# Performance work log

Hardware: AMD Instinct MI355X
Metric: run time of the kernel (lower is better)

The kernel has to match this reference:

```python
import jax, jax.numpy as jnp
import numpy as np
from jax import lax

B = 32      # point clouds per batch
P = 1024    # points per cloud (equal-sized, contiguous in batch vector)
K = 20      # kNN neighbors (includes self, as in PyG knn)
N = B * P


def _w(key, fan_in, fan_out):
    return jax.random.normal(key, (fan_in, fan_out), dtype=jnp.float32) / np.sqrt(fan_in)


def setup_inputs() -> dict:
    key = jax.random.key(0)
    ks = jax.random.split(key, 12)
    return {
        "pos": jax.random.normal(ks[0], (N, 3), dtype=jnp.float32),
        "batch": jnp.repeat(jnp.arange(B, dtype=jnp.int32), P),
        # conv1 MLP([6,64,64]): Linear(6,64)+BN+ReLU, Linear(64,64) plain
        "conv1_W1": _w(ks[1], 6, 64),
        "conv1_b1": jnp.zeros((64,), jnp.float32),
        "conv1_bn_scale": jnp.ones((64,), jnp.float32),   # BN eval folded affine
        "conv1_bn_bias": jnp.zeros((64,), jnp.float32),
        "conv1_W2": _w(ks[2], 64, 64),
        "conv1_b2": jnp.zeros((64,), jnp.float32),
        # conv2 MLP([128,128]): single plain Linear(128,128)
        "conv2_W": _w(ks[3], 128, 128),
        "conv2_b": jnp.zeros((128,), jnp.float32),
        # lin: Linear(64+128, 128)
        "lin_W": _w(ks[4], 192, 128),
        "lin_b": jnp.zeros((128,), jnp.float32),
    }


def _edge_conv(x, mlp_fn):
    # x: [B, P, d]. Dynamic kNN in feature space per cloud, edge MLP, max-aggregate.
    sq = jnp.sum(x * x, axis=-1)                                  # [B,P]
    dist = sq[:, :, None] - 2.0 * jnp.einsum('bpd,bqd->bpq', x, x) + sq[:, None, :]
    _, idx = lax.top_k(-dist, K)                                  # [B,P,K] nearest (incl. self)
    x_j = jax.vmap(lambda xb, ib: xb[ib])(x, idx)                 # [B,P,K,d] gather neighbors
    x_i = jnp.broadcast_to(x[:, :, None, :], x_j.shape)
    e = jnp.concatenate([x_i, x_j - x_i], axis=-1)                # [B,P,K,2d]
    return jnp.max(mlp_fn(e), axis=2)                             # max aggregation -> [B,P,out]


def reference(pos, batch, conv1_W1, conv1_b1, conv1_bn_scale, conv1_bn_bias,
              conv1_W2, conv1_b2, conv2_W, conv2_b, lin_W, lin_b):
    x = pos.reshape(B, P, 3)

    def mlp1(e):
        h = e @ conv1_W1 + conv1_b1
        h = jax.nn.relu(h * conv1_bn_scale + conv1_bn_bias)       # BN(eval) + ReLU
        return h @ conv1_W2 + conv1_b2                            # plain last layer

    def mlp2(e):
        return e @ conv2_W + conv2_b                              # plain single layer

    x1 = _edge_conv(x, mlp1)                                      # [B,P,64]
    x2 = _edge_conv(x1, mlp2)                                     # [B,P,128]
    h = jnp.concatenate([x1, x2], axis=-1) @ lin_W + lin_b        # [B,P,128]
    # global_max_pool over each cloud via batch ids
    out = jax.ops.segment_max(h.reshape(N, 128), batch, num_segments=B)
    return out                                                    # [B,128]
```

## Files before the change

kernel.cpp:

```cpp
#include <hip/hip_runtime.h>
#include <math.h>

#define NPTS 32768
#define NB 32
#define PP 1024
#define KK 20

using bf16x8 = __attribute__((ext_vector_type(8))) short;
using f32x4 = __attribute__((ext_vector_type(4))) float;

constexpr size_t OFF_X1 = 0;
constexpr size_t OFF_IDX = OFF_X1 + (size_t)NPTS * 64 * 4;
constexpr size_t OFF_U = OFF_IDX + (size_t)NPTS * KK * 4;
constexpr size_t OFF_V = OFF_U + (size_t)NPTS * 128 * 4;
constexpr size_t OFF_X2 = OFF_V + (size_t)NPTS * 128 * 4;
constexpr size_t OFF_H = OFF_X2 + (size_t)NPTS * 128 * 4;
constexpr size_t OFF_PART = OFF_H + (size_t)NPTS * 128 * 4;
constexpr size_t OFF_SQN = OFF_PART + (size_t)32 * 8 * 128 * 4;

__device__ __forceinline__ void topk_insert(unsigned (&l)[KK], unsigned key) {
#pragma unroll
  for (int j = KK - 1; j >= 1; --j) {
    unsigned r;
    asm("v_med3_u32 %0, %1, %2, %3" : "=v"(r) : "v"(key), "v"(l[j - 1]), "v"(l[j]));
    l[j] = r;
  }
  l[0] = key < l[0] ? key : l[0];
}

__device__ __forceinline__ unsigned pack_key(float dist, int q) {
  return (__float_as_uint(dist) & 0xFFFFFC00u) | (unsigned)q;
}

__device__ __forceinline__ void split_bf16(float x, short& hi, short& lo) {
  unsigned u = __float_as_uint(x);
  hi = (short)(u >> 16);
  float fh = __uint_as_float(u & 0xFFFF0000u);
  float r = x - fh;
  lo = (short)(__float_as_uint(r) >> 16);
}

template <int S>
__global__ __launch_bounds__(256, 4) void knn_topk3(const float* __restrict__ x,
                                                    unsigned* __restrict__ pk) {
  constexpr int CH = PP / S;
  __shared__ __align__(16) float xs[1024];
  __shared__ __align__(16) float ys[1024];
  __shared__ __align__(16) float zs[1024];
  int bx = blockIdx.x;
  int s = bx % S;
  int tile = (bx / S) % (PP / 256);
  int b = bx / (S * (PP / 256));
  int tid = threadIdx.x;
  const float* xb = x + (size_t)b * PP * 3;

  for (int t = tid; t < 768; t += 256) {
    float4 v = ((const float4*)xb)[t];
    int e = 4 * t;
    float vals[4] = {v.x, v.y, v.z, v.w};
#pragma unroll
    for (int j = 0; j < 4; ++j) {
      int p = (e + j) / 3, d = (e + j) % 3;
      if (d == 0) xs[p] = vals[j];
      else if (d == 1) ys[p] = vals[j];
      else zs[p] = vals[j];
    }
  }
  __syncthreads();

  int i = tile * 256 + tid;
  float xi0 = xs[i], xi1 = ys[i], xi2 = zs[i];

  unsigned l[KK];
#pragma unroll
  for (int j = 0; j < KK; ++j) l[j] = 0xFFFFFFFFu;

  int q0 = s * CH;
  float4 qx = *(const float4*)&xs[q0];
  float4 qy = *(const float4*)&ys[q0];
  float4 qz = *(const float4*)&zs[q0];
  for (int c = 0; c < CH; c += 4) {
    int qm = (q0 + c + 4) & 1023;
    float4 nqx = *(const float4*)&xs[qm];
    float4 nqy = *(const float4*)&ys[qm];
    float4 nqz = *(const float4*)&zs[qm];
    float cx[4] = {qx.x, qx.y, qx.z, qx.w};
    float cy[4] = {qy.x, qy.y, qy.z, qy.w};
    float cz[4] = {qz.x, qz.y, qz.z, qz.w};
#pragma unroll
    for (int j = 0; j < 4; ++j) {
      float d0 = xi0 - cx[j], d1 = xi1 - cy[j], d2 = xi2 - cz[j];
      float dist = fmaf(d0, d0, fmaf(d1, d1, d2 * d2));
      topk_insert(l, pack_key(dist, q0 + c + j));
    }
    qx = nqx; qy = nqy; qz = nqz;
  }
  size_t base = ((size_t)b * PP + i) * S + s;
#pragma unroll
  for (int j = 0; j < KK; ++j) pk[base * KK + j] = l[j];
}

template <int S>
__global__ __launch_bounds__(256) void knn_merge(const unsigned* __restrict__ pk,
                                                 int* __restrict__ idx_out) {
  int p = blockIdx.x * 256 + threadIdx.x;
  const unsigned* g = pk + (size_t)p * S * KK;
  unsigned l[KK];
#pragma unroll
  for (int j = 0; j < KK; ++j) l[j] = g[j];
  for (int s = 1; s < S; ++s) {
    const unsigned* gs = g + s * KK;
#pragma unroll
    for (int j = 0; j < KK; ++j) topk_insert(l, gs[j]);
  }
#pragma unroll
  for (int j = 0; j < KK; ++j) idx_out[(size_t)p * KK + j] = (int)(l[j] & 1023u);
}

__global__ __launch_bounds__(256) void precompute1(const float* __restrict__ pos,
                                                   const float* __restrict__ W1,
                                                   const float* __restrict__ b1,
                                                   float* __restrict__ u1,
                                                   float* __restrict__ v1) {
  int gid = blockIdx.x * 256 + threadIdx.x;
  int i = gid >> 6, c = gid & 63;
  float p0 = pos[(size_t)i * 3 + 0], p1 = pos[(size_t)i * 3 + 1], p2 = pos[(size_t)i * 3 + 2];
  float a0 = W1[0 * 64 + c], a1 = W1[1 * 64 + c], a2 = W1[2 * 64 + c];
  float g0 = W1[3 * 64 + c], g1 = W1[4 * 64 + c], g2 = W1[5 * 64 + c];
  float v = fmaf(p0, g0, fmaf(p1, g1, p2 * g2));
  float u = b1[c];
  u = fmaf(p0, a0 - g0, u);
  u = fmaf(p1, a1 - g1, u);
  u = fmaf(p2, a2 - g2, u);
  u1[gid] = u;
  v1[gid] = v;
}

__global__ __launch_bounds__(256) void edge_conv1_mfma(
    const float* __restrict__ u1, const float* __restrict__ v1,
    const int* __restrict__ idx, const float* __restrict__ W2,
    const float* __restrict__ scale, const float* __restrict__ bias,
    const float* __restrict__ b2,
    short* __restrict__ x1hl, float* __restrict__ sqn) {
  __shared__ float Cs[160 * 68];
  __shared__ int jt[160];
  __shared__ float xs[512];
  int tid = threadIdx.x;
  int p0 = blockIdx.x * 8;
  int b = p0 >> 10;
  if (tid < 160) {
    int e = tid;
    int i = p0 + e / 20;
    jt[e] = (b << 10) + idx[(size_t)i * KK + e % 20];
  }
  int w = tid >> 6, l = tid & 63, quad = l >> 4, lm = l & 15;
  int kq = quad * 8;
  float4 s00 = *(const float4*)(scale + kq);
  float4 s01 = *(const float4*)(scale + kq + 4);
  float4 s10 = *(const float4*)(scale + 32 + kq);
  float4 s11 = *(const float4*)(scale + 32 + kq + 4);
  float4 c00 = *(const float4*)(bias + kq);
  float4 c01 = *(const float4*)(bias + kq + 4);
  float4 c10 = *(const float4*)(bias + 32 + kq);
  float4 c11 = *(const float4*)(bias + 32 + kq + 4);
  bf16x8 Bh[4][2], Bl[4][2];
#pragma unroll
  for (int nt = 0; nt < 4; ++nt) {
#pragma unroll
    for (int ks = 0; ks < 2; ++ks) {
#pragma unroll
      for (int jj = 0; jj < 8; ++jj) {
        float wv = W2[(size_t)(ks * 32 + kq + jj) * 64 + nt * 16 + lm];
        short hi, lo;
        split_bf16(wv, hi, lo);
        Bh[nt][ks][jj] = hi;
        Bl[nt][ks][jj] = lo;
      }
    }
  }
  __syncthreads();

  for (int s = w; s < 10; s += 4) {
    f32x4 acc[4];
#pragma unroll
    for (int nt = 0; nt < 4; ++nt) acc[nt] = (f32x4){0.f, 0.f, 0.f, 0.f};
    int e = s * 16 + lm;
    int p = e / 20;
    int jrow = jt[e];
    const float* urow = u1 + (size_t)(p0 + p) * 64;
    const float* vrow = v1 + (size_t)jrow * 64;
#pragma unroll
    for (int ks = 0; ks < 2; ++ks) {
      int koff = ks * 32 + kq;
      float4 va = *(const float4*)(vrow + koff);
      float4 vb = *(const float4*)(vrow + koff + 4);
      float4 ua = *(const float4*)(urow + koff);
      float4 ub = *(const float4*)(urow + koff + 4);
      float4 sA = ks ? s10 : s00, sB = ks ? s11 : s01;
      float4 cA = ks ? c10 : c00, cB = ks ? c11 : c01;
      float hv[8];
      hv[0] = fmaxf(fmaf(ua.x + va.x, sA.x, cA.x), 0.f);
      hv[1] = fmaxf(fmaf(ua.y + va.y, sA.y, cA.y), 0.f);
      hv[2] = fmaxf(fmaf(ua.z + va.z, sA.z, cA.z), 0.f);
      hv[3] = fmaxf(fmaf(ua.w + va.w, sA.w, cA.w), 0.f);
      hv[4] = fmaxf(fmaf(ub.x + vb.x, sB.x, cB.x), 0.f);
      hv[5] = fmaxf(fmaf(ub.y + vb.y, sB.y, cB.y), 0.f);
      hv[6] = fmaxf(fmaf(ub.z + vb.z, sB.z, cB.z), 0.f);
      hv[7] = fmaxf(fmaf(ub.w + vb.w, sB.w, cB.w), 0.f);
      bf16x8 Ah, Al;
#pragma unroll
      for (int jj = 0; jj < 8; ++jj) {
        short hi, lo;
        split_bf16(hv[jj], hi, lo);
        Ah[jj] = hi;
        Al[jj] = lo;
      }
#pragma unroll
      for (int nt = 0; nt < 4; ++nt) {
        acc[nt] = __builtin_amdgcn_mfma_f32_16x16x32_bf16(Ah, Bh[nt][ks], acc[nt], 0, 0, 0);
        acc[nt] = __builtin_amdgcn_mfma_f32_16x16x32_bf16(Al, Bh[nt][ks], acc[nt], 0, 0, 0);
        acc[nt] = __builtin_amdgcn_mfma_f32_16x16x32_bf16(Ah, Bl[nt][ks], acc[nt], 0, 0, 0);
      }
    }
#pragma unroll
    for (int nt = 0; nt < 4; ++nt) {
#pragma unroll
      for (int r = 0; r < 4; ++r) {
        Cs[(size_t)(s * 16 + quad * 4 + r) * 68 + nt * 16 + lm] = acc[nt][r];
      }
    }
  }
  __syncthreads();
  for (int o = tid; o < 512; o += 256) {
    int p = o >> 6, c = o & 63;
    float m = -__builtin_inff();
    for (int k = 0; k < KK; ++k) m = fmaxf(m, Cs[(size_t)(p * 20 + k) * 68 + c]);
    m += b2[c];
    size_t gi = (size_t)(p0 + p) * 128 + c;
    short hi, lo;
    split_bf16(m, hi, lo);
    x1hl[gi] = hi;
    x1hl[gi + 64] = lo;
    xs[o] = m;
  }
  __syncthreads();
  if (tid < 8) {
    float ss = 0.f;
    for (int c = 0; c < 64; ++c) {
      float v = xs[tid * 64 + c];
      ss = fmaf(v, v, ss);
    }
    sqn[p0 + tid] = ss;
  }
}

__global__ __launch_bounds__(256, 4) void knn2_mfma(const short* __restrict__ x1hl,
                                                    const float* __restrict__ sqn,
                                                    unsigned* __restrict__ pk) {
  __shared__ float sqs[1024];
  int bx = blockIdx.x;
  int s = bx & 1;
  int pb = bx >> 1;
  int p0 = pb * 64;
  int b = p0 >> 10;
  int tid = threadIdx.x;
  for (int t = tid; t < 1024; t += 256) sqs[t] = sqn[(size_t)b * PP + t];
  int w = tid >> 6, l = tid & 63, quad = l >> 4, lm = l & 15;
  size_t gi = (size_t)p0 + w * 16 + lm;
  const short* brow = x1hl + gi * 128 + quad * 8;
  bf16x8 Bh0 = *(const bf16x8*)(brow);
  bf16x8 Bl0 = *(const bf16x8*)(brow + 64);
  bf16x8 Bh1 = *(const bf16x8*)(brow + 32);
  bf16x8 Bl1 = *(const bf16x8*)(brow + 96);
  float sqi = sqn[gi];
  __syncthreads();
  unsigned list[KK];
#pragma unroll
  for (int j = 0; j < KK; ++j) list[j] = 0xFFFFFFFFu;

  const size_t cbase = (size_t)b * PP;
  int m0 = s * 512;
  const short* arow = x1hl + (cbase + m0 + lm) * 128 + quad * 8;
  bf16x8 Ah0 = *(const bf16x8*)(arow);
  bf16x8 Al0 = *(const bf16x8*)(arow + 64);
  bf16x8 Ah1 = *(const bf16x8*)(arow + 32);
  bf16x8 Al1 = *(const bf16x8*)(arow + 96);
  float sq0 = sqs[m0 + quad * 4 + 0];
  float sq1 = sqs[m0 + quad * 4 + 1];
  float sq2 = sqs[m0 + quad * 4 + 2];
  float sq3 = sqs[m0 + quad * 4 + 3];

  for (int it = 0; it < 32; ++it) {
    int m0n = (m0 + 16) & 1023;
    const short* arn = x1hl + (cbase + m0n + lm) * 128 + quad * 8;
    bf16x8 nAh0 = *(const bf16x8*)(arn);
    bf16x8 nAl0 = *(const bf16x8*)(arn + 64);
    bf16x8 nAh1 = *(const bf16x8*)(arn + 32);
    bf16x8 nAl1 = *(const bf16x8*)(arn + 96);
    float nsq0 = sqs[m0n + quad * 4 + 0];
    float nsq1 = sqs[m0n + quad * 4 + 1];
    float nsq2 = sqs[m0n + quad * 4 + 2];
    float nsq3 = sqs[m0n + quad * 4 + 3];

    f32x4 acc = (f32x4){0.f, 0.f, 0.f, 0.f};
    acc = __builtin_amdgcn_mfma_f32_16x16x32_bf16(Ah0, Bh0, acc, 0, 0, 0);
    acc = __builtin_amdgcn_mfma_f32_16x16x32_bf16(Al0, Bh0, acc, 0, 0, 0);
    acc = __builtin_amdgcn_mfma_f32_16x16x32_bf16(Ah0, Bl0, acc, 0, 0, 0);
    acc = __builtin_amdgcn_mfma_f32_16x16x32_bf16(Ah1, Bh1, acc, 0, 0, 0);
    acc = __builtin_amdgcn_mfma_f32_16x16x32_bf16(Al1, Bh1, acc, 0, 0, 0);
    acc = __builtin_amdgcn_mfma_f32_16x16x32_bf16(Ah1, Bl1, acc, 0, 0, 0);

    int qb = m0 + quad * 4;
    float d0 = fmaxf(0.f, fmaf(-2.f, acc[0], sqi + sq0));
    topk_insert(list, pack_key(d0, qb + 0));
    float d1 = fmaxf(0.f, fmaf(-2.f, acc[1], sqi + sq1));
    topk_insert(list, pack_key(d1, qb + 1));
    float d2 = fmaxf(0.f, fmaf(-2.f, acc[2], sqi + sq2));
    topk_insert(list, pack_key(d2, qb + 2));
    float d3 = fmaxf(0.f, fmaf(-2.f, acc[3], sqi + sq3));
    topk_insert(list, pack_key(d3, qb + 3));

    Ah0 = nAh0; Al0 = nAl0; Ah1 = nAh1; Al1 = nAl1;
    sq0 = nsq0; sq1 = nsq1; sq2 = nsq2; sq3 = nsq3;
    m0 += 16;
  }
  unsigned sub = s * 4 + quad;
  unsigned* dst = pk + ((size_t)gi * 8 + sub) * KK;
#pragma unroll
  for (int j = 0; j < KK; ++j) dst[j] = list[j];
}

__global__ __launch_bounds__(256) void pre2_mfma(const short* __restrict__ x1hl,
                                                 const float* __restrict__ cW,
                                                 const float* __restrict__ cb,
                                                 float* __restrict__ u2,
                                                 float* __restrict__ v2) {
  constexpr int BS = 72;
  __shared__ short Bh[128 * BS];
  __shared__ short Bl[128 * BS];
  int tid = threadIdx.x;
  int nh = blockIdx.x & 1;
  int p0 = (blockIdx.x >> 1) * 64;
  for (int t = tid; t < 64 * 128; t += 256) {
    int k = t >> 7, n = t & 127;
    float wb_ = cW[(size_t)(64 + k) * 128 + n];
    float wv = nh ? wb_ : (cW[(size_t)k * 128 + n] - wb_);
    short hi, lo;
    split_bf16(wv, hi, lo);
    Bh[n * BS + k] = hi;
    Bl[n * BS + k] = lo;
  }
  __syncthreads();
  int w = tid >> 6, l = tid & 63, quad = l >> 4, lm = l & 15;
  int row = p0 + w * 16 + lm;
  f32x4 acc[8];
#pragma unroll
  for (int nt = 0; nt < 8; ++nt) acc[nt] = (f32x4){0.f, 0.f, 0.f, 0.f};
#pragma unroll
  for (int ks = 0; ks < 2; ++ks) {
    int kb = ks * 32 + quad * 8;
    bf16x8 Ah = *(const bf16x8*)(x1hl + (size_t)row * 128 + kb);
    bf16x8 Al = *(const bf16x8*)(x1hl + (size_t)row * 128 + 64 + kb);
#pragma unroll
    for (int nt = 0; nt < 8; ++nt) {
      bf16x8 Wh = *(const bf16x8*)(Bh + (nt * 16 + lm) * BS + kb);
      bf16x8 Wl = *(const bf16x8*)(Bl + (nt * 16 + lm) * BS + kb);
      acc[nt] = __builtin_amdgcn_mfma_f32_16x16x32_bf16(Ah, Wh, acc[nt], 0, 0, 0);
      acc[nt] = __builtin_amdgcn_mfma_f32_16x16x32_bf16(Al, Wh, acc[nt], 0, 0, 0);
      acc[nt] = __builtin_amdgcn_mfma_f32_16x16x32_bf16(Ah, Wl, acc[nt], 0, 0, 0);
    }
  }
  float* out = nh ? v2 : u2;
  int prow = p0 + w * 16 + quad * 4;
#pragma unroll
  for (int nt = 0; nt < 8; ++nt) {
    int col = nt * 16 + lm;
    float bias = nh ? 0.f : cb[col];
#pragma unroll
    for (int r = 0; r < 4; ++r)
      out[(size_t)(prow + r) * 128 + col] = acc[nt][r] + bias;
  }
}

__global__ __launch_bounds__(256) void gathermax2(const float* __restrict__ u2,
                                                  const float* __restrict__ v2,
                                                  const int* __restrict__ idx,
                                                  short* __restrict__ x2hl) {
  int gid = blockIdx.x * 256 + threadIdx.x;
  int i = gid >> 7, c = gid & 127;
  int b = i >> 10;
  const int* myidx = idx + (size_t)i * KK;
  float m = -__builtin_inff();
  for (int k = 0; k < KK; ++k) {
    int j = (b << 10) + myidx[k];
    m = fmaxf(m, v2[(size_t)j * 128 + c]);
  }
  float x = u2[gid] + m;
  short hi, lo;
  split_bf16(x, hi, lo);
  x2hl[(size_t)i * 256 + c] = hi;
  x2hl[(size_t)i * 256 + 128 + c] = lo;
}

__global__ __launch_bounds__(256) void lin_mfma(const short* __restrict__ x1hl,
                                                const short* __restrict__ x2hl,
                                                const float* __restrict__ LW,
                                                const float* __restrict__ lb,
                                                float* __restrict__ h) {
  constexpr int BS = 200;
  __shared__ short Bh[64 * BS];
  __shared__ short Bl[64 * BS];
  int tid = threadIdx.x;
  int nh = blockIdx.x & 1;
  int p0 = (blockIdx.x >> 1) * 64;
  for (int t = tid; t < 192 * 64; t += 256) {
    int k = t >> 6, n = t & 63;
    float wv = LW[(size_t)k * 128 + nh * 64 + n];
    short hi, lo;
    split_bf16(wv, hi, lo);
    Bh[n * BS + k] = hi;
    Bl[n * BS + k] = lo;
  }
  __syncthreads();
  int w = tid >> 6, l = tid & 63, quad = l >> 4, lm = l & 15;
  int row = p0 + w * 16 + lm;
  f32x4 acc[4];
#pragma unroll
  for (int nt = 0; nt < 4; ++nt) acc[nt] = (f32x4){0.f, 0.f, 0.f, 0.f};
#pragma unroll
  for (int ks = 0; ks < 6; ++ks) {
    int kb = ks * 32 + quad * 8;
    bf16x8 Ah, Al;
    if (ks < 2) {
      Ah = *(const bf16x8*)(x1hl + (size_t)row * 128 + kb);
      Al = *(const bf16x8*)(x1hl + (size_t)row * 128 + 64 + kb);
    } else {
      Ah = *(const bf16x8*)(x2hl + (size_t)row * 256 + (kb - 64));
      Al = *(const bf16x8*)(x2hl + (size_t)row * 256 + 128 + (kb - 64));
    }
#pragma unroll
    for (int nt = 0; nt < 4; ++nt) {
      bf16x8 Wh = *(const bf16x8*)(Bh + (nt * 16 + lm) * BS + kb);
      bf16x8 Wl = *(const bf16x8*)(Bl + (nt * 16 + lm) * BS + kb);
      acc[nt] = __builtin_amdgcn_mfma_f32_16x16x32_bf16(Ah, Wh, acc[nt], 0, 0, 0);
      acc[nt] = __builtin_amdgcn_mfma_f32_16x16x32_bf16(Al, Wh, acc[nt], 0, 0, 0);
      acc[nt] = __builtin_amdgcn_mfma_f32_16x16x32_bf16(Ah, Wl, acc[nt], 0, 0, 0);
    }
  }
  int prow = p0 + w * 16 + quad * 4;
#pragma unroll
  for (int nt = 0; nt < 4; ++nt) {
    int col = nh * 64 + nt * 16 + lm;
    float bias = lb[col];
#pragma unroll
    for (int r = 0; r < 4; ++r)
      h[(size_t)(prow + r) * 128 + col] = acc[nt][r] + bias;
  }
}

__global__ __launch_bounds__(128) void segmax_a(const float* __restrict__ h,
                                                float* __restrict__ part) {
  int b = blockIdx.x >> 3, chunk = blockIdx.x & 7;
  int c = threadIdx.x;
  float m = -__builtin_inff();
  for (int p = 0; p < 128; ++p) {
    size_t i = (size_t)b * PP + chunk * 128 + p;
    m = fmaxf(m, h[i * 128 + c]);
  }
  part[(size_t)blockIdx.x * 128 + c] = m;
}

__global__ __launch_bounds__(128) void segmax_b(const float* __restrict__ part,
                                                float* __restrict__ out) {
  int b = blockIdx.x;
  int c = threadIdx.x;
  float m = -__builtin_inff();
  for (int k = 0; k < 8; ++k) m = fmaxf(m, part[((size_t)b * 8 + k) * 128 + c]);
  out[(size_t)b * 128 + c] = m;
}

extern "C" void kernel_launch(void* const* d_in, const int* in_sizes, int n_in,
                              void* d_out, int out_size, void* d_ws, size_t ws_size,
                              hipStream_t stream) {
  const float* pos = (const float*)d_in[0];
  const float* W1 = (const float*)d_in[2];
  const float* b1 = (const float*)d_in[3];
  const float* bn_s = (const float*)d_in[4];
  const float* bn_b = (const float*)d_in[5];
  const float* W2 = (const float*)d_in[6];
  const float* b2 = (const float*)d_in[7];
  const float* cW = (const float*)d_in[8];
  const float* cb = (const float*)d_in[9];
  const float* LW = (const float*)d_in[10];
  const float* lb = (const float*)d_in[11];
  float* out = (float*)d_out;

  char* ws = (char*)d_ws;
  short* x1hl = (short*)(ws + OFF_X1);
  int* idx = (int*)(ws + OFF_IDX);
  float* u1 = (float*)(ws + OFF_U);
  float* v1 = (float*)(ws + OFF_V);
  float* u2 = (float*)(ws + OFF_U);
  float* v2 = (float*)(ws + OFF_V);
  short* x2hl = (short*)(ws + OFF_X2);
  float* hbuf = (float*)(ws + OFF_H);
  float* part = (float*)(ws + OFF_PART);
  float* sqn = (float*)(ws + OFF_SQN);
  unsigned* pk = (unsigned*)(ws + OFF_U);

  knn_topk3<8><<<NB * 4 * 8, 256, 0, stream>>>(pos, pk);
  knn_merge<8><<<NPTS / 256, 256, 0, stream>>>(pk, idx);
  precompute1<<<NPTS * 64 / 256, 256, 0, stream>>>(pos, W1, b1, u1, v1);
  edge_conv1_mfma<<<NPTS / 8, 256, 0, stream>>>(u1, v1, idx, W2, bn_s, bn_b, b2,
                                                x1hl, sqn);
  knn2_mfma<<<NPTS / 64 * 2, 256, 0, stream>>>(x1hl, sqn, pk);
  knn_merge<8><<<NPTS / 256, 256, 0, stream>>>(pk, idx);
  pre2_mfma<<<NPTS / 64 * 2, 256, 0, stream>>>(x1hl, cW, cb, u2, v2);
  gathermax2<<<NPTS * 128 / 256, 256, 0, stream>>>(u2, v2, idx, x2hl);
  lin_mfma<<<NPTS / 64 * 2, 256, 0, stream>>>(x1hl, x2hl, LW, lb, hbuf);
  segmax_a<<<NB * 8, 128, 0, stream>>>(hbuf, part);
  segmax_b<<<NB, 128, 0, stream>>>(part, out);
}
```

Measured before the change: 344.6 us.

## Split per-thread top-k into two independent lists and stage knn2 tiles in LDS

Both kNN kernels now keep two independent top-20 lists per thread, each fed alternate candidates. This breaks the serial med3 insertion dependency chain and gives the scheduler more instruction-level parallelism. knn2 stages 128-row bf16 hi/lo tiles of candidate features in shared memory instead of loading per-lane from global memory. The merge kernel now reduces 16 partial lists and exits early once a sorted partial list's next key cannot enter the current list. The costs are more registers, double the partial-list traffic and a longer merge.

```diff
diff --git a/kernel.cpp b/kernel.cpp
--- a/kernel.cpp
+++ b/kernel.cpp
@@ -71,9 +71,9 @@
   int i = tile * 256 + tid;
   float xi0 = xs[i], xi1 = ys[i], xi2 = zs[i];
 
-  unsigned l[KK];
-#pragma unroll
-  for (int j = 0; j < KK; ++j) l[j] = 0xFFFFFFFFu;
+  unsigned la[KK], lb[KK];
+#pragma unroll
+  for (int j = 0; j < KK; ++j) { la[j] = 0xFFFFFFFFu; lb[j] = 0xFFFFFFFFu; }
 
   int q0 = s * CH;
   float4 qx = *(const float4*)&xs[q0];
@@ -87,17 +87,29 @@
     float cx[4] = {qx.x, qx.y, qx.z, qx.w};
     float cy[4] = {qy.x, qy.y, qy.z, qy.w};
     float cz[4] = {qz.x, qz.y, qz.z, qz.w};
-#pragma unroll
-    for (int j = 0; j < 4; ++j) {
-      float d0 = xi0 - cx[j], d1 = xi1 - cy[j], d2 = xi2 - cz[j];
-      float dist = fmaf(d0, d0, fmaf(d1, d1, d2 * d2));
-      topk_insert(l, pack_key(dist, q0 + c + j));
+    {
+      float d0 = xi0 - cx[0], d1 = xi1 - cy[0], d2 = xi2 - cz[0];
+      topk_insert(la, pack_key(fmaf(d0, d0, fmaf(d1, d1, d2 * d2)), q0 + c + 0));
+    }
+    {
+      float d0 = xi0 - cx[2], d1 = xi1 - cy[2], d2 = xi2 - cz[2];
+      topk_insert(lb, pack_key(fmaf(d0, d0, fmaf(d1, d1, d2 * d2)), q0 + c + 2));
+    }
+    {
+      float d0 = xi0 - cx[1], d1 = xi1 - cy[1], d2 = xi2 - cz[1];
+      topk_insert(la, pack_key(fmaf(d0, d0, fmaf(d1, d1, d2 * d2)), q0 + c + 1));
+    }
+    {
+      float d0 = xi0 - cx[3], d1 = xi1 - cy[3], d2 = xi2 - cz[3];
+      topk_insert(lb, pack_key(fmaf(d0, d0, fmaf(d1, d1, d2 * d2)), q0 + c + 3));
     }
     qx = nqx; qy = nqy; qz = nqz;
   }
-  size_t base = ((size_t)b * PP + i) * S + s;
-#pragma unroll
-  for (int j = 0; j < KK; ++j) pk[base * KK + j] = l[j];
+  size_t base = ((size_t)b * PP + i) * (2 * S) + s * 2;
+#pragma unroll
+  for (int j = 0; j < KK; ++j) pk[base * KK + j] = la[j];
+#pragma unroll
+  for (int j = 0; j < KK; ++j) pk[(base + 1) * KK + j] = lb[j];
 }
 
 template <int S>
@@ -110,8 +122,11 @@
   for (int j = 0; j < KK; ++j) l[j] = g[j];
   for (int s = 1; s < S; ++s) {
     const unsigned* gs = g + s * KK;
-#pragma unroll
-    for (int j = 0; j < KK; ++j) topk_insert(l, gs[j]);
+    for (int j = 0; j < KK; ++j) {
+      unsigned key = gs[j];
+      if (key >= l[KK - 1]) break;
+      topk_insert(l, key);
+    }
   }
 #pragma unroll
   for (int j = 0; j < KK; ++j) idx_out[(size_t)p * KK + j] = (int)(l[j] & 1023u);
@@ -257,14 +272,17 @@
 __global__ __launch_bounds__(256, 4) void knn2_mfma(const short* __restrict__ x1hl,
                                                     const float* __restrict__ sqn,
                                                     unsigned* __restrict__ pk) {
-  __shared__ float sqs[1024];
+  constexpr int TS = 72;
+  __shared__ float sqs[512];
+  __shared__ __align__(16) short tileH[128 * TS];
+  __shared__ __align__(16) short tileL[128 * TS];
   int bx = blockIdx.x;
   int s = bx & 1;
   int pb = bx >> 1;
   int p0 = pb * 64;
   int b = p0 >> 10;
   int tid = threadIdx.x;
-  for (int t = tid; t < 1024; t += 256) sqs[t] = sqn[(size_t)b * PP + t];
+  for (int t = tid; t < 512; t += 256) sqs[t] = sqn[(size_t)b * PP + s * 512 + t];
   int w = tid >> 6, l = tid & 63, quad = l >> 4, lm = l & 15;
   size_t gi = (size_t)p0 + w * 16 + lm;
   const short* brow = x1hl + gi * 128 + quad * 8;
@@ -273,61 +291,61 @@
   bf16x8 Bh1 = *(const bf16x8*)(brow + 32);
   bf16x8 Bl1 = *(const bf16x8*)(brow + 96);
   float sqi = sqn[gi];
-  __syncthreads();
-  unsigned list[KK];
-#pragma unroll
-  for (int j = 0; j < KK; ++j) list[j] = 0xFFFFFFFFu;
-
-  const size_t cbase = (size_t)b * PP;
-  int m0 = s * 512;
-  const short* arow = x1hl + (cbase + m0 + lm) * 128 + quad * 8;
-  bf16x8 Ah0 = *(const bf16x8*)(arow);
-  bf16x8 Al0 = *(const bf16x8*)(arow + 64);
-  bf16x8 Ah1 = *(const bf16x8*)(arow + 32);
-  bf16x8 Al1 = *(const bf16x8*)(arow + 96);
-  float sq0 = sqs[m0 + quad * 4 + 0];
-  float sq1 = sqs[m0 + quad * 4 + 1];
-  float sq2 = sqs[m0 + quad * 4 + 2];
-  float sq3 = sqs[m0 + quad * 4 + 3];
-
-  for (int it = 0; it < 32; ++it) {
-    int m0n = (m0 + 16) & 1023;
-    const short* arn = x1hl + (cbase + m0n + lm) * 128 + quad * 8;
-    bf16x8 nAh0 = *(const bf16x8*)(arn);
-    bf16x8 nAl0 = *(const bf16x8*)(arn + 64);
-    bf16x8 nAh1 = *(const bf16x8*)(arn + 32);
-    bf16x8 nAl1 = *(const bf16x8*)(arn + 96);
-    float nsq0 = sqs[m0n + quad * 4 + 0];
-    float nsq1 = sqs[m0n + quad * 4 + 1];
-    float nsq2 = sqs[m0n + quad * 4 + 2];
-    float nsq3 = sqs[m0n + quad * 4 + 3];
-
-    f32x4 acc = (f32x4){0.f, 0.f, 0.f, 0.f};
-    acc = __builtin_amdgcn_mfma_f32_16x16x32_bf16(Ah0, Bh0, acc, 0, 0, 0);
-    acc = __builtin_amdgcn_mfma_f32_16x16x32_bf16(Al0, Bh0, acc, 0, 0, 0);
-    acc = __builtin_amdgcn_mfma_f32_16x16x32_bf16(Ah0, Bl0, acc, 0, 0, 0);
-    acc = __builtin_amdgcn_mfma_f32_16x16x32_bf16(Ah1, Bh1, acc, 0, 0, 0);
-    acc = __builtin_amdgcn_mfma_f32_16x16x32_bf16(Al1, Bh1, acc, 0, 0, 0);
-    acc = __builtin_amdgcn_mfma_f32_16x16x32_bf16(Ah1, Bl1, acc, 0, 0, 0);
-
-    int qb = m0 + quad * 4;
-    float d0 = fmaxf(0.f, fmaf(-2.f, acc[0], sqi + sq0));
-    topk_insert(list, pack_key(d0, qb + 0));
-    float d1 = fmaxf(0.f, fmaf(-2.f, acc[1], sqi + sq1));
-    topk_insert(list, pack_key(d1, qb + 1));
-    float d2 = fmaxf(0.f, fmaf(-2.f, acc[2], sqi + sq2));
-    topk_insert(list, pack_key(d2, qb + 2));
-    float d3 = fmaxf(0.f, fmaf(-2.f, acc[3], sqi + sq3));
-    topk_insert(list, pack_key(d3, qb + 3));
-
-    Ah0 = nAh0; Al0 = nAl0; Ah1 = nAh1; Al1 = nAl1;
-    sq0 = nsq0; sq1 = nsq1; sq2 = nsq2; sq3 = nsq3;
-    m0 += 16;
-  }
-  unsigned sub = s * 4 + quad;
-  unsigned* dst = pk + ((size_t)gi * 8 + sub) * KK;
-#pragma unroll
-  for (int j = 0; j < KK; ++j) dst[j] = list[j];
+
+  unsigned la[KK], lc[KK];
+#pragma unroll
+  for (int j = 0; j < KK; ++j) { la[j] = 0xFFFFFFFFu; lc[j] = 0xFFFFFFFFu; }
+
+  int rr = tid & 127, hh = tid >> 7;
+  short* dstT = (hh ? tileL : tileH) + rr * TS;
+  const size_t cbase = (size_t)b * PP + s * 512;
+  const short* srcbase = x1hl + (cbase + rr) * 128 + hh * 64;
+
+  for (int tile = 0; tile < 4; ++tile) {
+    __syncthreads();
+    {
+      const short* src = srcbase + (size_t)tile * 128 * 128;
+#pragma unroll
+      for (int j = 0; j < 8; ++j)
+        *(bf16x8*)(dstT + j * 8) = *(const bf16x8*)(src + j * 8);
+    }
+    __syncthreads();
+#pragma unroll
+    for (int it = 0; it < 8; ++it) {
+      int row = it * 16 + lm;
+      const short* aH = tileH + row * TS + quad * 8;
+      const short* aL = tileL + row * TS + quad * 8;
+      bf16x8 Ah0 = *(const bf16x8*)(aH);
+      bf16x8 Ah1 = *(const bf16x8*)(aH + 32);
+      bf16x8 Al0 = *(const bf16x8*)(aL);
+      bf16x8 Al1 = *(const bf16x8*)(aL + 32);
+
+      f32x4 acc = (f32x4){0.f, 0.f, 0.f, 0.f};
+      acc = __builtin_amdgcn_mfma_f32_16x16x32_bf16(Ah0, Bh0, acc, 0, 0, 0);
+      acc = __builtin_amdgcn_mfma_f32_16x16x32_bf16(Al0, Bh0, acc, 0, 0, 0);
+      acc = __builtin_amdgcn_mfma_f32_16x16x32_bf16(Ah0, Bl0, acc, 0, 0, 0);
+      acc = __builtin_amdgcn_mfma_f32_16x16x32_bf16(Ah1, Bh1, acc, 0, 0, 0);
+      acc = __builtin_amdgcn_mfma_f32_16x16x32_bf16(Al1, Bh1, acc, 0, 0, 0);
+      acc = __builtin_amdgcn_mfma_f32_16x16x32_bf16(Ah1, Bl1, acc, 0, 0, 0);
+
+      int qloc = tile * 128 + it * 16 + quad * 4;
+      int qg = s * 512 + qloc;
+      float d0 = fmaxf(0.f, fmaf(-2.f, acc[0], sqi + sqs[qloc + 0]));
+      float d2 = fmaxf(0.f, fmaf(-2.f, acc[2], sqi + sqs[qloc + 2]));
+      topk_insert(la, pack_key(d0, qg + 0));
+      topk_insert(lc, pack_key(d2, qg + 2));
+      float d1 = fmaxf(0.f, fmaf(-2.f, acc[1], sqi + sqs[qloc + 1]));
+      float d3 = fmaxf(0.f, fmaf(-2.f, acc[3], sqi + sqs[qloc + 3]));
+      topk_insert(la, pack_key(d1, qg + 1));
+      topk_insert(lc, pack_key(d3, qg + 3));
+    }
+  }
+  unsigned sub = (unsigned)(s * 4 + quad) * 2;
+  unsigned* dst = pk + ((size_t)gi * 16 + sub) * KK;
+#pragma unroll
+  for (int j = 0; j < KK; ++j) dst[j] = la[j];
+#pragma unroll
+  for (int j = 0; j < KK; ++j) dst[KK + j] = lc[j];
 }
 
 __global__ __launch_bounds__(256) void pre2_mfma(const short* __restrict__ x1hl,
@@ -509,12 +527,12 @@
   unsigned* pk = (unsigned*)(ws + OFF_U);
 
   knn_topk3<8><<<NB * 4 * 8, 256, 0, stream>>>(pos, pk);
-  knn_merge<8><<<NPTS / 256, 256, 0, stream>>>(pk, idx);
+  knn_merge<16><<<NPTS / 256, 256, 0, stream>>>(pk, idx);
   precompute1<<<NPTS * 64 / 256, 256, 0, stream>>>(pos, W1, b1, u1, v1);
   edge_conv1_mfma<<<NPTS / 8, 256, 0, stream>>>(u1, v1, idx, W2, bn_s, bn_b, b2,
                                                 x1hl, sqn);
   knn2_mfma<<<NPTS / 64 * 2, 256, 0, stream>>>(x1hl, sqn, pk);
-  knn_merge<8><<<NPTS / 256, 256, 0, stream>>>(pk, idx);
+  knn_merge<16><<<NPTS / 256, 256, 0, stream>>>(pk, idx);
   pre2_mfma<<<NPTS / 64 * 2, 256, 0, stream>>>(x1hl, cW, cb, u2, v2);
   gathermax2<<<NPTS * 128 / 256, 256, 0, stream>>>(u2, v2, idx, x2hl);
   lin_mfma<<<NPTS / 64 * 2, 256, 0, stream>>>(x1hl, x2hl, LW, lb, hbuf);
```

Result: slower. 377.0 us (+9.4%).
